# Kernel optimization log

Measured on AMD Instinct MI355X. Metric: run time of the kernel, lower is better.

Reference implementation:

```python
import jax, jax.numpy as jnp
import numpy as np

E = 512
H = 8
D = E // H
WIN = 128  # mask_window_size


def setup_inputs() -> dict:
    key = jax.random.key(0)
    k1, k2, k3, k4, k5 = jax.random.split(key, 5)
    B, L = 2, 4096
    s = 1.0 / np.sqrt(E)
    return {
        "x": jax.random.normal(k1, (B, L, E), dtype=jnp.float32),
        "in_proj_w": jax.random.normal(k2, (3 * E, E), dtype=jnp.float32) * s,
        "in_proj_b": jax.random.normal(k3, (3 * E,), dtype=jnp.float32) * 0.02,
        "out_w": jax.random.normal(k4, (E, E), dtype=jnp.float32) * s,
        "out_b": jax.random.normal(k5, (E,), dtype=jnp.float32) * 0.02,
    }


def reference(x, in_proj_w, in_proj_b, out_w, out_b):
    B, L, _ = x.shape
    # fused qkv projection (torch MultiheadAttention in_proj): x @ W.T + b
    qkv = jnp.einsum("ble,fe->blf", x, in_proj_w) + in_proj_b  # [B,L,3E]
    q, k, v = jnp.split(qkv, 3, axis=-1)
    # [B,H,L,D]
    q = q.reshape(B, L, H, D).transpose(0, 2, 1, 3)
    k = k.reshape(B, L, H, D).transpose(0, 2, 1, 3)
    v = v.reshape(B, L, H, D).transpose(0, 2, 1, 3)
    scores = jnp.einsum("bhqd,bhkd->bhqk", q, k) / jnp.sqrt(jnp.float32(D))
    # (diagonal stays blocked — faithful to the original gen_mask quirk)
    idx = jnp.arange(L)
    dist = jnp.abs(idx[:, None] - idx[None, :])
    blocked = (dist > WIN) | (dist == 0)  # [L,L]
    scores = jnp.where(blocked[None, None], -jnp.inf, scores)
    attn = jax.nn.softmax(scores, axis=-1)  # [B,H,L,L]
    out = jnp.einsum("bhqk,bhkd->bhqd", attn, v)  # [B,H,L,D]
    out = out.transpose(0, 2, 1, 3).reshape(B, L, E)
    return jnp.einsum("ble,fe->blf", out, out_w) + out_b
```

## Files before the change

kernel.cpp:

```cpp
#include <hip/hip_runtime.h>
#include <math.h>

#define E_DIM 512
#define H_DIM 8
#define WIN 128
#define L_SEQ 4096
#define B_SZ 2

typedef unsigned short ushort_t;
typedef unsigned int uint_t;
typedef __attribute__((ext_vector_type(8))) __bf16 bf16x8;
typedef __attribute__((ext_vector_type(4))) float f32x4;

__device__ __forceinline__ ushort_t f2bf(float f) {
    uint_t u = __float_as_uint(f);
    u = u + 0x7fffu + ((u >> 16) & 1u);
    return (ushort_t)(u >> 16);
}
__device__ __forceinline__ float bf2f(ushort_t h) {
    return __uint_as_float((uint_t)h << 16);
}

__device__ __forceinline__ void gload16(const ushort_t* g, ushort_t* l) {
    __builtin_amdgcn_global_load_lds(
        (const __attribute__((address_space(1))) void*)g,
        (__attribute__((address_space(3))) void*)l,
        16, 0, 0);
}


__global__ __launch_bounds__(256) void convertX(
    const float* __restrict__ x,  ushort_t* __restrict__ xh,
    const float* __restrict__ w1, ushort_t* __restrict__ w1h, ushort_t* __restrict__ w1l,
    const float* __restrict__ w2, ushort_t* __restrict__ w2h, ushort_t* __restrict__ w2l) {
    int sg = blockIdx.x * 256 + threadIdx.x;
    const float* src; ushort_t* dh; ushort_t* dl; bool wantLo;
    if (sg < 524288)      { src = x;  dh = xh;  dl = nullptr; wantLo = false; }
    else if (sg < 622592) { src = w1; dh = w1h; dl = w1l; wantLo = true; sg -= 524288; }
    else                  { src = w2; dh = w2h; dl = w2l; wantLo = true; sg -= 622592; }
    const int tile = sg >> 6, slot = sg & 63;
    const int row = (tile >> 4) * 16 + (slot & 15);
    const int k   = (tile & 15) * 32 + (slot >> 4) * 8;
    const float4 v0 = *(const float4*)&src[(size_t)row * 512 + k];
    const float4 v1 = *(const float4*)&src[(size_t)row * 512 + k + 4];
    const float vv[8] = {v0.x, v0.y, v0.z, v0.w, v1.x, v1.y, v1.z, v1.w};
    union { ushort_t u[8]; ushort4 v[2]; } h, l;
    #pragma unroll
    for (int j = 0; j < 8; j++) {
        const ushort_t a = f2bf(vv[j]);
        h.u[j] = a;
        l.u[j] = f2bf(vv[j] - bf2f(a));
    }
    ((ushort4*)(dh + (size_t)sg * 8))[0] = h.v[0];
    ((ushort4*)(dh + (size_t)sg * 8))[1] = h.v[1];
    if (wantLo) {
        ((ushort4*)(dl + (size_t)sg * 8))[0] = l.v[0];
        ((ushort4*)(dl + (size_t)sg * 8))[1] = l.v[1];
    }
}

__global__ __launch_bounds__(256) void gemm_qkv(
    const ushort_t* __restrict__ Ah,
    const ushort_t* __restrict__ Wh, const ushort_t* __restrict__ Wl,
    const float* __restrict__ bias,
    ushort_t* __restrict__ qTh, ushort_t* __restrict__ qTl,
    ushort_t* __restrict__ kTh, ushort_t* __restrict__ kTl,
    ushort_t* __restrict__ vTh) {
    __shared__ __align__(16) ushort_t sAh[16 * 512];
    __shared__ __align__(16) ushort_t sWh[16 * 512];
    __shared__ __align__(16) ushort_t sWl[16 * 512];

    const int tid = threadIdx.x, lane = tid & 63, w = tid >> 6;
    const int wm = w & 1, wn = w >> 1, ln = lane & 15, quad = lane >> 4;
    const int bx = blockIdx.x, by = blockIdx.y;
    const int lo8 = lane * 8;
    const int wu = __builtin_amdgcn_readfirstlane(w);

    f32x4 acc[4][4];
    const f32x4 zero = {0.f, 0.f, 0.f, 0.f};
    #pragma unroll
    for (int i = 0; i < 4; i++)
        #pragma unroll
        for (int j = 0; j < 4; j++) acc[i][j] = zero;

    const ushort_t* pb[12];
    ushort_t* db[12];
    #pragma unroll
    for (int t = 0; t < 12; t++) {
        const int g = wu * 12 + t;
        if (g < 16) {
            pb[t] = Ah + ((size_t)(bx * 8 + (g >> 1)) * 16 + (g & 1)) * 512;
            db[t] = &sAh[g * 512];
        } else if (g < 32) {
            const int u = g - 16;
            pb[t] = Wh + ((size_t)(by * 8 + (u >> 1)) * 16 + (u & 1)) * 512;
            db[t] = &sWh[u * 512];
        } else {
            const int u = g - 32;
            pb[t] = Wl + ((size_t)(by * 8 + (u >> 1)) * 16 + (u & 1)) * 512;
            db[t] = &sWl[u * 512];
        }
    }

    for (int KT = 0; KT < 8; KT++) {
        const int koff = KT * 1024;
        __syncthreads();
        #pragma unroll
        for (int t = 0; t < 12; t++)
            gload16(pb[t] + koff + lo8, db[t]);
        __syncthreads();

        #pragma unroll
        for (int ks = 0; ks < 2; ks++) {
            bf16x8 fah[4];
            #pragma unroll
            for (int i = 0; i < 4; i++)
                fah[i] = *(const bf16x8*)&sAh[((wm * 4 + i) * 2 + ks) * 512 + lo8];
            #pragma unroll
            for (int j = 0; j < 4; j++) {
                const bf16x8 fbh = *(const bf16x8*)&sWh[((wn * 4 + j) * 2 + ks) * 512 + lo8];
                const bf16x8 fbl = *(const bf16x8*)&sWl[((wn * 4 + j) * 2 + ks) * 512 + lo8];
                #pragma unroll
                for (int i = 0; i < 4; i++) {
                    acc[i][j] = __builtin_amdgcn_mfma_f32_16x16x32_bf16(fah[i], fbh, acc[i][j], 0, 0, 0);
                    acc[i][j] = __builtin_amdgcn_mfma_f32_16x16x32_bf16(fah[i], fbl, acc[i][j], 0, 0, 0);
                }
            }
        }
    }

    const int b = bx >> 5;
    const int h = 2 * (by & 3) + wn;
    if (by < 8) {
        ushort_t* dh = (by < 4) ? qTh : kTh;
        ushort_t* dl = (by < 4) ? qTl : kTl;
        #pragma unroll
        for (int i = 0; i < 4; i++) {
            const int rt = (bx & 31) * 8 + wm * 4 + i;
            const size_t tb = ((size_t)(b * 8 + h) * 256 + rt) * 2;
            #pragma unroll
            for (int j = 0; j < 4; j++) {
                const float bv = bias[by * 128 + wn * 64 + j * 16 + ln];
                const size_t tile = tb + (j >> 1);
                #pragma unroll
                for (int r = 0; r < 4; r++) {
                    const int slot = ((j * 2 + (ln >> 3)) & 3) * 16 + quad * 4 + r;
                    const size_t idx = tile * 512 + slot * 8 + (ln & 7);
                    const float v = acc[i][j][r] + bv;
                    const ushort_t hh = f2bf(v);
                    dh[idx] = hh;
                    dl[idx] = f2bf(v - bf2f(hh));
                }
            }
        }
    } else {
        const int kwin = (bx & 31) * 2 + wm;
        #pragma unroll
        for (int i = 0; i < 4; i++) {
            const int kk = i >> 1;
            #pragma unroll
            for (int j = 0; j < 4; j++) {
                const float bv = bias[by * 128 + wn * 64 + j * 16 + ln];
                const size_t tile = (((size_t)(b * 8 + h) * 64 + kwin) * 4 + j) * 2 + kk;
                #pragma unroll
                for (int r = 0; r < 4; r++) {
                    const int klq = quad * 4 + r;
                    const int slot = ((i & 1) * 2 + (klq >> 3)) * 16 + ln;
                    const size_t idx = tile * 512 + slot * 8 + (klq & 7);
                    vTh[idx] = f2bf(acc[i][j][r] + bv);
                }
            }
        }
    }
}

__global__ __launch_bounds__(512) void attn_mfma(
    const ushort_t* __restrict__ qTh, const ushort_t* __restrict__ qTl,
    const ushort_t* __restrict__ kTh, const ushort_t* __restrict__ kTl,
    const ushort_t* __restrict__ vTh,
    ushort_t* __restrict__ outh) {
    __shared__ __align__(16) ushort_t sKh[8 * 512];
    __shared__ __align__(16) ushort_t sKl[8 * 512];
    __shared__ __align__(16) ushort_t sV [8 * 512];
    __shared__ __align__(16) ushort_t sP [16 * 512];

    const int qs = blockIdx.x * 128;
    const int h = blockIdx.y, b = blockIdx.z;
    const int bh = b * 8 + h;
    const int tid = threadIdx.x, lane = tid & 63;
    const int w = tid >> 6, ln = lane & 15, quad = lane >> 4;
    const int lo8 = lane * 8;

    bf16x8 qf[2][2];
    {
        const size_t qt = ((size_t)bh * 256 + (qs >> 4) + w) * 2;
        qf[0][0] = *(const bf16x8*)(qTh + (qt + 0) * 512 + lo8);
        qf[1][0] = *(const bf16x8*)(qTh + (qt + 1) * 512 + lo8);
        qf[0][1] = *(const bf16x8*)(qTl + (qt + 0) * 512 + lo8);
        qf[1][1] = *(const bf16x8*)(qTl + (qt + 1) * 512 + lo8);
    }

    f32x4 oacc[4];
    const f32x4 zero = {0.f, 0.f, 0.f, 0.f};
    #pragma unroll
    for (int dt = 0; dt < 4; dt++) oacc[dt] = zero;
    float m_run[4], l_run[4];
    #pragma unroll
    for (int r = 0; r < 4; r++) { m_run[r] = -1e30f; l_run[r] = 0.f; }

    const float cscale = 0.125f * 1.44269504f;
    const int qlo = qs + 16 * w;

    for (int kt = 0; kt < 6; kt++) {
        const int ks = qs - 128 + kt * 64;

        __syncthreads();

        if (w < 4) {
            int st = (qs >> 4) - 8 + kt * 4 + w;
            st = st < 0 ? 0 : (st > 255 ? 255 : st);
            const size_t kb = ((size_t)bh * 256 + st) * 2 * 512 + lo8;
            gload16(kTh + kb,       &sKh[(w * 2 + 0) * 512]);
            gload16(kTh + kb + 512, &sKh[(w * 2 + 1) * 512]);
            gload16(kTl + kb,       &sKl[(w * 2 + 0) * 512]);
            gload16(kTl + kb + 512, &sKl[(w * 2 + 1) * 512]);
        } else {
            const int u = w - 4;
            int vw = (qs >> 6) - 2 + kt;
            vw = vw < 0 ? 0 : (vw > 63 ? 63 : vw);
            const size_t vb = (((size_t)bh * 64 + vw) * 4 + u) * 2 * 512 + lo8;
            gload16(vTh + vb,       &sV[(u * 2 + 0) * 512]);
            gload16(vTh + vb + 512, &sV[(u * 2 + 1) * 512]);
        }
        __syncthreads();

        f32x4 sacc[4];
        #pragma unroll
        for (int jt = 0; jt < 4; jt++) {
            f32x4 a = zero;
            const int klo = ks + 16 * jt;
            const bool dead = (klo > qlo + 15 + WIN) || (klo + 15 < qlo - WIN) ||
                              (klo >= L_SEQ) || (klo + 15 < 0);
            if (!dead) {
                #pragma unroll
                for (int kk = 0; kk < 2; kk++) {
                    const bf16x8 kh = *(const bf16x8*)&sKh[(jt * 2 + kk) * 512 + lo8];
                    const bf16x8 klo2 = *(const bf16x8*)&sKl[(jt * 2 + kk) * 512 + lo8];
                    a = __builtin_amdgcn_mfma_f32_16x16x32_bf16(qf[kk][0], kh, a, 0, 0, 0);
                    a = __builtin_amdgcn_mfma_f32_16x16x32_bf16(qf[kk][0], klo2, a, 0, 0, 0);
                    a = __builtin_amdgcn_mfma_f32_16x16x32_bf16(qf[kk][1], kh, a, 0, 0, 0);
                }
            }
            sacc[jt] = a;
        }

        float u[4][4];
        #pragma unroll
        for (int jt = 0; jt < 4; jt++) {
            const int kcol = ks + 16 * jt + ln;
            #pragma unroll
            for (int r = 0; r < 4; r++) {
                const int qrow = qlo + quad * 4 + r;
                const int dist = qrow > kcol ? qrow - kcol : kcol - qrow;
                const bool ok = (kcol >= 0) && (kcol < L_SEQ) && (dist >= 1) && (dist <= WIN);
                u[jt][r] = ok ? sacc[jt][r] * cscale : -INFINITY;
            }
        }
        float mk[4];
        #pragma unroll
        for (int r = 0; r < 4; r++)
            mk[r] = fmaxf(fmaxf(u[0][r], u[1][r]), fmaxf(u[2][r], u[3][r]));
        #pragma unroll
        for (int off = 1; off <= 8; off <<= 1)
            #pragma unroll
            for (int r = 0; r < 4; r++)
                mk[r] = fmaxf(mk[r], __shfl_xor(mk[r], off));

        float alpha[4], psum[4], p[4][4];
        #pragma unroll
        for (int r = 0; r < 4; r++) {
            const float mnew = fmaxf(fmaxf(m_run[r], mk[r]), -1e30f);
            alpha[r] = exp2f(m_run[r] - mnew);
            m_run[r] = mnew;
            psum[r] = 0.f;
            #pragma unroll
            for (int jt = 0; jt < 4; jt++) {
                p[jt][r] = exp2f(u[jt][r] - mnew);
                psum[r] += p[jt][r];
            }
        }
        #pragma unroll
        for (int off = 1; off <= 8; off <<= 1)
            #pragma unroll
            for (int r = 0; r < 4; r++)
                psum[r] += __shfl_xor(psum[r], off);
        #pragma unroll
        for (int r = 0; r < 4; r++)
            l_run[r] = l_run[r] * alpha[r] + psum[r];

        #pragma unroll
        for (int dt = 0; dt < 4; dt++)
            #pragma unroll
            for (int r = 0; r < 4; r++)
                oacc[dt][r] *= alpha[r];

        #pragma unroll
        for (int jt = 0; jt < 4; jt++)
            #pragma unroll
            for (int r = 0; r < 4; r++) {
                const int slot = ((jt & 1) * 2 + (ln >> 3)) * 16 + quad * 4 + r;
                sP[w * 1024 + (jt >> 1) * 512 + slot * 8 + (ln & 7)] = f2bf(p[jt][r]);
            }

        #pragma unroll
        for (int kk = 0; kk < 2; kk++) {
            const bf16x8 pf = *(const bf16x8*)&sP[w * 1024 + kk * 512 + lo8];
            #pragma unroll
            for (int dt = 0; dt < 4; dt++) {
                const bf16x8 vf = *(const bf16x8*)&sV[(dt * 2 + kk) * 512 + lo8];
                oacc[dt] = __builtin_amdgcn_mfma_f32_16x16x32_bf16(pf, vf, oacc[dt], 0, 0, 0);
            }
        }
    }

    const int Rt = ((b * L_SEQ + qs) >> 4) + w;
    #pragma unroll
    for (int r = 0; r < 4; r++) {
        const float inv_l = 1.f / l_run[r];
        #pragma unroll
        for (int dt = 0; dt < 4; dt++) {
            const float v = oacc[dt][r] * inv_l;
            const int tile = Rt * 16 + h * 2 + (dt >> 1);
            const int slot = ((dt & 1) * 2 + (ln >> 3)) * 16 + quad * 4 + r;
            const size_t idx = (size_t)tile * 512 + slot * 8 + (ln & 7);
            outh[idx] = f2bf(v);
        }
    }
}

__global__ __launch_bounds__(512) void gemm_out(
    const ushort_t* __restrict__ Ah,
    const ushort_t* __restrict__ Wh, const ushort_t* __restrict__ Wl,
    const float* __restrict__ bias, float* __restrict__ C) {
    __shared__ __align__(16) ushort_t sAh[16 * 512];
    __shared__ __align__(16) ushort_t sWh[8 * 512];
    __shared__ __align__(16) ushort_t sWl[8 * 512];

    const int tid = threadIdx.x, lane = tid & 63, w = tid >> 6;
    const int wm = w & 3, wn = w >> 2, ln = lane & 15, quad = lane >> 4;
    const int bx = blockIdx.x, by = blockIdx.y;
    const int lo8 = lane * 8;
    const int wu = __builtin_amdgcn_readfirstlane(w);

    f32x4 acc[2][2];
    const f32x4 zero = {0.f, 0.f, 0.f, 0.f};
    #pragma unroll
    for (int i = 0; i < 2; i++)
        #pragma unroll
        for (int j = 0; j < 2; j++) acc[i][j] = zero;

    const ushort_t* pb[4];
    ushort_t* db[4];
    #pragma unroll
    for (int t = 0; t < 4; t++) {
        const int g = wu * 4 + t;
        if (g < 16) {
            pb[t] = Ah + ((size_t)(bx * 8 + (g >> 1)) * 16 + (g & 1)) * 512;
            db[t] = &sAh[g * 512];
        } else if (g < 24) {
            const int u = g - 16;
            pb[t] = Wh + ((size_t)(by * 4 + (u >> 1)) * 16 + (u & 1)) * 512;
            db[t] = &sWh[u * 512];
        } else {
            const int u = g - 24;
            pb[t] = Wl + ((size_t)(by * 4 + (u >> 1)) * 16 + (u & 1)) * 512;
            db[t] = &sWl[u * 512];
        }
    }

    for (int KT = 0; KT < 8; KT++) {
        const int koff = KT * 1024;
        __syncthreads();
        #pragma unroll
        for (int t = 0; t < 4; t++)
            gload16(pb[t] + koff + lo8, db[t]);
        __syncthreads();

        #pragma unroll
        for (int ks = 0; ks < 2; ks++) {
            bf16x8 fah[2];
            #pragma unroll
            for (int i = 0; i < 2; i++)
                fah[i] = *(const bf16x8*)&sAh[((wm * 2 + i) * 2 + ks) * 512 + lo8];
            #pragma unroll
            for (int j = 0; j < 2; j++) {
                const bf16x8 fbh = *(const bf16x8*)&sWh[((wn * 2 + j) * 2 + ks) * 512 + lo8];
                const bf16x8 fbl = *(const bf16x8*)&sWl[((wn * 2 + j) * 2 + ks) * 512 + lo8];
                #pragma unroll
                for (int i = 0; i < 2; i++) {
                    acc[i][j] = __builtin_amdgcn_mfma_f32_16x16x32_bf16(fah[i], fbh, acc[i][j], 0, 0, 0);
                    acc[i][j] = __builtin_amdgcn_mfma_f32_16x16x32_bf16(fah[i], fbl, acc[i][j], 0, 0, 0);
                }
            }
        }
    }

    #pragma unroll
    for (int i = 0; i < 2; i++) {
        const int row0 = bx * 128 + wm * 32 + i * 16 + quad * 4;
        #pragma unroll
        for (int j = 0; j < 2; j++) {
            const int col = by * 64 + wn * 32 + j * 16 + ln;
            const float bv = bias[col];
            #pragma unroll
            for (int r = 0; r < 4; r++)
                C[(size_t)(row0 + r) * E_DIM + col] = acc[i][j][r] + bv;
        }
    }
}

extern "C" void kernel_launch(void* const* d_in, const int* in_sizes, int n_in,
                              void* d_out, int out_size, void* d_ws, size_t ws_size,
                              hipStream_t stream) {
    const float* x         = (const float*)d_in[0];
    const float* in_proj_w = (const float*)d_in[1];
    const float* in_proj_b = (const float*)d_in[2];
    const float* out_w     = (const float*)d_in[3];
    const float* out_b     = (const float*)d_in[4];
    float* out = (float*)d_out;

    const int N = B_SZ * L_SEQ;
    const size_t NE = (size_t)N * E_DIM;

    char* p = (char*)d_ws;
    ushort_t* xh  = (ushort_t*)p; p += NE * 2;
    ushort_t* w1h = (ushort_t*)p; p += (size_t)3 * E_DIM * E_DIM * 2;
    ushort_t* w1l = (ushort_t*)p; p += (size_t)3 * E_DIM * E_DIM * 2;
    ushort_t* w2h = (ushort_t*)p; p += (size_t)E_DIM * E_DIM * 2;
    ushort_t* w2l = (ushort_t*)p; p += (size_t)E_DIM * E_DIM * 2;
    ushort_t* qTh = (ushort_t*)p; p += NE * 2;
    ushort_t* qTl = (ushort_t*)p; p += NE * 2;
    ushort_t* kTh = (ushort_t*)p; p += NE * 2;
    ushort_t* kTl = (ushort_t*)p; p += NE * 2;
    ushort_t* vTh = (ushort_t*)p; p += NE * 2;
    ushort_t* ath = (ushort_t*)p; p += NE * 2;

    convertX<<<2560, 256, 0, stream>>>(x, xh, in_proj_w, w1h, w1l, out_w, w2h, w2l);

    gemm_qkv<<<dim3(64, 12), 256, 0, stream>>>(
        xh, w1h, w1l, in_proj_b, qTh, qTl, kTh, kTl, vTh);

    attn_mfma<<<dim3(L_SEQ / 128, H_DIM, B_SZ), 512, 0, stream>>>(
        qTh, qTl, kTh, kTl, vTh, ath);

    gemm_out<<<dim3(64, 8), 512, 0, stream>>>(
        ath, w2h, w2l, out_b, out);
}
```

Measured before the change: 156.3 us.

## Double-buffer LDS tiles in QKV and output GEMMs to overlap loads with MFMA

Both projection GEMMs switch to ping-pong shared-memory buffers. The first K-tile is prefetched before the loop, and each iteration issues the next tile's global-to-LDS loads before computing on the current buffer, which cuts the barriers per iteration from two to one. The QKV kernel also moves to 16 thinner K-steps so its LDS footprint stays the same. The output GEMM doubles its LDS use, which may lower occupancy, and the gain depends on the compiler not forcing a full vmcnt wait before the LDS reads.

```diff
diff --git a/kernel.cpp b/kernel.cpp
--- a/kernel.cpp
+++ b/kernel.cpp
@@ -66,9 +66,9 @@
     ushort_t* __restrict__ qTh, ushort_t* __restrict__ qTl,
     ushort_t* __restrict__ kTh, ushort_t* __restrict__ kTl,
     ushort_t* __restrict__ vTh) {
-    __shared__ __align__(16) ushort_t sAh[16 * 512];
-    __shared__ __align__(16) ushort_t sWh[16 * 512];
-    __shared__ __align__(16) ushort_t sWl[16 * 512];
+    __shared__ __align__(16) ushort_t sAh[2][8 * 512];
+    __shared__ __align__(16) ushort_t sWh[2][8 * 512];
+    __shared__ __align__(16) ushort_t sWl[2][8 * 512];
 
     const int tid = threadIdx.x, lane = tid & 63, w = tid >> 6;
     const int wm = w & 1, wn = w >> 1, ln = lane & 15, quad = lane >> 4;
@@ -83,48 +83,55 @@
         #pragma unroll
         for (int j = 0; j < 4; j++) acc[i][j] = zero;
 
-    const ushort_t* pb[12];
-    ushort_t* db[12];
-    #pragma unroll
-    for (int t = 0; t < 12; t++) {
-        const int g = wu * 12 + t;
-        if (g < 16) {
-            pb[t] = Ah + ((size_t)(bx * 8 + (g >> 1)) * 16 + (g & 1)) * 512;
-            db[t] = &sAh[g * 512];
-        } else if (g < 32) {
+    const ushort_t* pb[6];
+    ushort_t* db0[6];
+    ushort_t* db1[6];
+    #pragma unroll
+    for (int t = 0; t < 6; t++) {
+        const int g = wu * 6 + t;
+        if (g < 8) {
+            pb[t] = Ah + ((size_t)(bx * 8 + g) * 16) * 512;
+            db0[t] = &sAh[0][g * 512]; db1[t] = &sAh[1][g * 512];
+        } else if (g < 16) {
+            const int u = g - 8;
+            pb[t] = Wh + ((size_t)(by * 8 + u) * 16) * 512;
+            db0[t] = &sWh[0][u * 512]; db1[t] = &sWh[1][u * 512];
+        } else {
             const int u = g - 16;
-            pb[t] = Wh + ((size_t)(by * 8 + (u >> 1)) * 16 + (u & 1)) * 512;
-            db[t] = &sWh[u * 512];
-        } else {
-            const int u = g - 32;
-            pb[t] = Wl + ((size_t)(by * 8 + (u >> 1)) * 16 + (u & 1)) * 512;
-            db[t] = &sWl[u * 512];
-        }
-    }
-
-    for (int KT = 0; KT < 8; KT++) {
-        const int koff = KT * 1024;
+            pb[t] = Wl + ((size_t)(by * 8 + u) * 16) * 512;
+            db0[t] = &sWl[0][u * 512]; db1[t] = &sWl[1][u * 512];
+        }
+    }
+
+    #pragma unroll
+    for (int t = 0; t < 6; t++)
+        gload16(pb[t] + lo8, db0[t]);
+
+    for (int kt = 0; kt < 16; kt++) {
         __syncthreads();
-        #pragma unroll
-        for (int t = 0; t < 12; t++)
-            gload16(pb[t] + koff + lo8, db[t]);
-        __syncthreads();
-
-        #pragma unroll
-        for (int ks = 0; ks < 2; ks++) {
-            bf16x8 fah[4];
-            #pragma unroll
-            for (int i = 0; i < 4; i++)
-                fah[i] = *(const bf16x8*)&sAh[((wm * 4 + i) * 2 + ks) * 512 + lo8];
-            #pragma unroll
-            for (int j = 0; j < 4; j++) {
-                const bf16x8 fbh = *(const bf16x8*)&sWh[((wn * 4 + j) * 2 + ks) * 512 + lo8];
-                const bf16x8 fbl = *(const bf16x8*)&sWl[((wn * 4 + j) * 2 + ks) * 512 + lo8];
-                #pragma unroll
-                for (int i = 0; i < 4; i++) {
-                    acc[i][j] = __builtin_amdgcn_mfma_f32_16x16x32_bf16(fah[i], fbh, acc[i][j], 0, 0, 0);
-                    acc[i][j] = __builtin_amdgcn_mfma_f32_16x16x32_bf16(fah[i], fbl, acc[i][j], 0, 0, 0);
-                }
+        if (kt < 15) {
+            const int koff = (kt + 1) * 512;
+            if ((kt + 1) & 1) {
+                #pragma unroll
+                for (int t = 0; t < 6; t++) gload16(pb[t] + koff + lo8, db1[t]);
+            } else {
+                #pragma unroll
+                for (int t = 0; t < 6; t++) gload16(pb[t] + koff + lo8, db0[t]);
+            }
+        }
+        const int cb = kt & 1;
+        bf16x8 fah[4];
+        #pragma unroll
+        for (int i = 0; i < 4; i++)
+            fah[i] = *(const bf16x8*)&sAh[cb][(wm * 4 + i) * 512 + lo8];
+        #pragma unroll
+        for (int j = 0; j < 4; j++) {
+            const bf16x8 fbh = *(const bf16x8*)&sWh[cb][(wn * 4 + j) * 512 + lo8];
+            const bf16x8 fbl = *(const bf16x8*)&sWl[cb][(wn * 4 + j) * 512 + lo8];
+            #pragma unroll
+            for (int i = 0; i < 4; i++) {
+                acc[i][j] = __builtin_amdgcn_mfma_f32_16x16x32_bf16(fah[i], fbh, acc[i][j], 0, 0, 0);
+                acc[i][j] = __builtin_amdgcn_mfma_f32_16x16x32_bf16(fah[i], fbl, acc[i][j], 0, 0, 0);
             }
         }
     }
@@ -342,9 +349,9 @@
     const ushort_t* __restrict__ Ah,
     const ushort_t* __restrict__ Wh, const ushort_t* __restrict__ Wl,
     const float* __restrict__ bias, float* __restrict__ C) {
-    __shared__ __align__(16) ushort_t sAh[16 * 512];
-    __shared__ __align__(16) ushort_t sWh[8 * 512];
-    __shared__ __align__(16) ushort_t sWl[8 * 512];
+    __shared__ __align__(16) ushort_t sAh[2][16 * 512];
+    __shared__ __align__(16) ushort_t sWh[2][8 * 512];
+    __shared__ __align__(16) ushort_t sWl[2][8 * 512];
 
     const int tid = threadIdx.x, lane = tid & 63, w = tid >> 6;
     const int wm = w & 3, wn = w >> 2, ln = lane & 15, quad = lane >> 4;
@@ -360,42 +367,52 @@
         for (int j = 0; j < 2; j++) acc[i][j] = zero;
 
     const ushort_t* pb[4];
-    ushort_t* db[4];
+    ushort_t* db0[4];
+    ushort_t* db1[4];
     #pragma unroll
     for (int t = 0; t < 4; t++) {
         const int g = wu * 4 + t;
         if (g < 16) {
             pb[t] = Ah + ((size_t)(bx * 8 + (g >> 1)) * 16 + (g & 1)) * 512;
-            db[t] = &sAh[g * 512];
+            db0[t] = &sAh[0][g * 512]; db1[t] = &sAh[1][g * 512];
         } else if (g < 24) {
             const int u = g - 16;
             pb[t] = Wh + ((size_t)(by * 4 + (u >> 1)) * 16 + (u & 1)) * 512;
-            db[t] = &sWh[u * 512];
+            db0[t] = &sWh[0][u * 512]; db1[t] = &sWh[1][u * 512];
         } else {
             const int u = g - 24;
             pb[t] = Wl + ((size_t)(by * 4 + (u >> 1)) * 16 + (u & 1)) * 512;
-            db[t] = &sWl[u * 512];
-        }
-    }
+            db0[t] = &sWl[0][u * 512]; db1[t] = &sWl[1][u * 512];
+        }
+    }
+
+    #pragma unroll
+    for (int t = 0; t < 4; t++)
+        gload16(pb[t] + lo8, db0[t]);
 
     for (int KT = 0; KT < 8; KT++) {
-        const int koff = KT * 1024;
         __syncthreads();
-        #pragma unroll
-        for (int t = 0; t < 4; t++)
-            gload16(pb[t] + koff + lo8, db[t]);
-        __syncthreads();
-
+        if (KT < 7) {
+            const int koff = (KT + 1) * 1024;
+            if ((KT + 1) & 1) {
+                #pragma unroll
+                for (int t = 0; t < 4; t++) gload16(pb[t] + koff + lo8, db1[t]);
+            } else {
+                #pragma unroll
+                for (int t = 0; t < 4; t++) gload16(pb[t] + koff + lo8, db0[t]);
+            }
+        }
+        const int cb = KT & 1;
         #pragma unroll
         for (int ks = 0; ks < 2; ks++) {
             bf16x8 fah[2];
             #pragma unroll
             for (int i = 0; i < 2; i++)
-                fah[i] = *(const bf16x8*)&sAh[((wm * 2 + i) * 2 + ks) * 512 + lo8];
+                fah[i] = *(const bf16x8*)&sAh[cb][((wm * 2 + i) * 2 + ks) * 512 + lo8];
             #pragma unroll
             for (int j = 0; j < 2; j++) {
-                const bf16x8 fbh = *(const bf16x8*)&sWh[((wn * 2 + j) * 2 + ks) * 512 + lo8];
-                const bf16x8 fbl = *(const bf16x8*)&sWl[((wn * 2 + j) * 2 + ks) * 512 + lo8];
+                const bf16x8 fbh = *(const bf16x8*)&sWh[cb][((wn * 2 + j) * 2 + ks) * 512 + lo8];
+                const bf16x8 fbl = *(const bf16x8*)&sWl[cb][((wn * 2 + j) * 2 + ks) * 512 + lo8];
                 #pragma unroll
                 for (int i = 0; i < 2; i++) {
                     acc[i][j] = __builtin_amdgcn_mfma_f32_16x16x32_bf16(fah[i], fbh, acc[i][j], 0, 0, 0);
```

After: 152.8 us. 1.02x faster.
